# Performance work log

Measured on AMD Instinct MI355X. Metric: run time of the kernel, lower is better.

## Reference

```python
import jax, jax.numpy as jnp
import numpy as np

K = 3; STRIDE = 1; PAD = 1; DIL = 1; KN = K * K * K  # num_pts = 27


def _trilinear_sample(vol, grid):
    """F.grid_sample 3D, mode=bilinear, padding=zeros, align_corners=False.
    vol: (C, D, H, W); grid: (od, oh, ow, 3) with xyz order in [-1, 1].
    Returns (C, od, oh, ow)."""
    C, D, H, W = vol.shape
    # unnormalize (align_corners=False)
    ix = ((grid[..., 0] + 1.0) * W - 1.0) * 0.5
    iy = ((grid[..., 1] + 1.0) * H - 1.0) * 0.5
    iz = ((grid[..., 2] + 1.0) * D - 1.0) * 0.5
    x0 = jnp.floor(ix); y0 = jnp.floor(iy); z0 = jnp.floor(iz)
    out = jnp.zeros((C,) + grid.shape[:-1], vol.dtype)
    for dz in (0, 1):
        for dy in (0, 1):
            for dx in (0, 1):
                xc = x0 + dx; yc = y0 + dy; zc = z0 + dz
                w = (1.0 - jnp.abs(ix - xc)) * (1.0 - jnp.abs(iy - yc)) * (1.0 - jnp.abs(iz - zc))
                valid = (xc >= 0) & (xc < W) & (yc >= 0) & (yc < H) & (zc >= 0) & (zc < D)
                xi = jnp.clip(xc, 0, W - 1).astype(jnp.int32)
                yi = jnp.clip(yc, 0, H - 1).astype(jnp.int32)
                zi = jnp.clip(zc, 0, D - 1).astype(jnp.int32)
                val = vol[:, zi, yi, xi]  # (C, od, oh, ow)
                out = out + val * (w * valid.astype(vol.dtype))[None]
    return out


def setup_inputs() -> dict:
    key = jax.random.key(0)
    k1, k2, k3 = jax.random.split(key, 3)
    N, C, D, H, W = 2, 64, 16, 32, 32
    inp = jax.random.normal(k1, (N, C, D, H, W), dtype=jnp.float32)
    offset = jax.random.normal(k2, (N, KN * 3, D, H, W), dtype=jnp.float32)
    weight = jax.random.normal(k3, (64, 64, KN), dtype=jnp.float32) * 0.05
    return {"input": inp, "offset": offset, "weight": weight}


def reference(input, offset, weight):
    N, C, D, H, W = input.shape
    od, oh, ow = offset.shape[2], offset.shape[3], offset.shape[4]
    f32 = input.dtype
    # base sampling mesh (align_corners=True style normalization, as original)
    z = (jnp.arange(od) * STRIDE - PAD + ((K - 1) // 2) * DIL).astype(f32)
    y = (jnp.arange(oh) * STRIDE - PAD + ((K - 1) // 2) * DIL).astype(f32)
    x = (jnp.arange(ow) * STRIDE - PAD + ((K - 1) // 2) * DIL).astype(f32)
    mz, my, mx = jnp.meshgrid(z, y, x, indexing="ij")
    norm = lambda v, S: (v - (S - 1) / 2.0) / ((S - 1) / 2.0)
    mesh = jnp.stack([norm(mx, W), norm(my, H), norm(mz, D)], axis=-1)  # (od,oh,ow,3)
    # offsets: channel layout per kernel point is (dz, dy, dx)
    off = offset.reshape(N, KN, 3, od, oh, ow)
    goff = jnp.stack([
        off[:, :, 2] / ((W - 1) / 2.0),
        off[:, :, 1] / ((H - 1) / 2.0),
        off[:, :, 0] / ((D - 1) / 2.0),
    ], axis=-1)  # (N, KN, od, oh, ow, 3) xyz
    grid = mesh[None, None] + goff
    # per-batch, per-kernel-point trilinear gather -> (N, KN, C, od, oh, ow)
    sampled = jax.vmap(lambda v, g: jax.vmap(lambda gg: _trilinear_sample(v, gg))(g))(input, grid)
    # grouped matmul: weight (O, C, KN) flattened C-major matches sampled layout
    out = jnp.einsum("ock,nkcdhw->nodhw", weight, sampled)
    return out
```

## Files before the change

kernel.cpp:

```cpp
#include <hip/hip_runtime.h>

typedef __attribute__((ext_vector_type(8))) _Float16 half8;
typedef __attribute__((ext_vector_type(4))) float floatx4;

constexpr int NB  = 2;
constexpr int CC  = 64;
constexpr int DD  = 16;
constexpr int HH  = 32;
constexpr int WW  = 32;
constexpr int KN_ = 27;
constexpr int OC  = 64;
constexpr int DHW = DD * HH * WW;
constexpr int TP  = 16;
constexpr int KCH = 9;

__device__ __forceinline__ unsigned short f2h(float f) {
    _Float16 h = (_Float16)f;
    return *(unsigned short*)&h;
}

__global__ __launch_bounds__(256) void k_prep(const float* __restrict__ in,
                                              const float* __restrict__ w,
                                              unsigned int* __restrict__ outu,
                                              unsigned short* __restrict__ wf) {
    int bid = blockIdx.x;
    int t = threadIdx.x;
    if (bid < 512) {
        __shared__ float tile[64][65];
        int n  = bid >> 8;
        int v0 = (bid & 255) << 6;
        int lane = t & 63, row = t >> 6;
#pragma unroll
        for (int i = 0; i < 16; ++i) {
            int c = (i << 2) + row;
            tile[c][lane] = in[(size_t)(n * CC + c) * DHW + v0 + lane];
        }
        __syncthreads();
#pragma unroll
        for (int i = 0; i < 8; ++i) {
            int flat = i * 256 + t;
            int v = flat >> 5, cd = flat & 31;
            unsigned int lo = f2h(tile[2 * cd][v]);
            unsigned int hi = f2h(tile[2 * cd + 1][v]);
            outu[(size_t)(n * DHW + v0 + v) * 32 + cd] = lo | (hi << 16);
        }
    } else {
        int f = (bid - 512) * 256 + t;
        int i  = f & 7;
        int l  = (f >> 3) & 63;
        int ot = (f >> 9) & 3;
        int cc = (f >> 11) & 1;
        int k  = f >> 12;
        int o = ot * 16 + (l & 15);
        int c = cc * 32 + ((l >> 4) << 3) + i;
        wf[f] = f2h(w[(o * CC + c) * KN_ + k]);
    }
}

__global__ __launch_bounds__(128, 6) void k_main(const unsigned short* __restrict__ inp,
                                                 const unsigned short* __restrict__ wf,
                                                 const float* __restrict__ offs,
                                                 float* __restrict__ out) {
    __shared__ unsigned short S[2 * TP * 64];
    __shared__ unsigned int   SU[KCH * TP * 12];

    int t   = threadIdx.x;
    int bid = blockIdx.x;
    int n   = (bid >> 2) & 1;
    int idx = ((bid >> 3) << 2) | (bid & 3);
    int p0  = idx << 4;

    int sp = t >> 3;
    int cg = t & 7;
    int wv = t >> 6, l = t & 63;
    int lrow = l & 15, lk = l >> 4;

    const float* offb = offs + (size_t)n * (3 * KN_) * DHW + p0;
    const char*  inb  = (const char*)(inp + ((size_t)n * DHW << 6));

    floatx4 acc0 = {0.f, 0.f, 0.f, 0.f};
    floatx4 acc1 = {0.f, 0.f, 0.f, 0.f};

    const int cgo   = cg << 4;
    const int woff  = sp * 64 + ((cg ^ (sp & 7)) << 3);
    const int roff0 = lrow * 64 + (((0 | lk) ^ (lrow & 7)) << 3);
    const int roff1 = lrow * 64 + (((4 | lk) ^ (lrow & 7)) << 3);

    for (int ch = 0; ch < 3; ++ch) {
        __syncthreads();

        for (int si = t; si < KCH * TP; si += 128) {
            int kk = si >> 4, p = si & 15;
            int k  = ch * KCH + kk;
            int pa = p0 + p;
            int dpos = pa >> 10, hpos = (pa >> 5) & 31, wpos = pa & 31;

            float oz = offb[(k * 3 + 0) * DHW + p];
            float oy = offb[(k * 3 + 1) * DHW + p];
            float ox = offb[(k * 3 + 2) * DHW + p];
            float ix = ((float)wpos + ox) * (32.0f / 31.0f) - 0.5f;
            float iy = ((float)hpos + oy) * (32.0f / 31.0f) - 0.5f;
            float iz = ((float)dpos + oz) * (16.0f / 15.0f) - 0.5f;
            float xf = floorf(ix), yf = floorf(iy), zf = floorf(iz);
            float fx = ix - xf, fy = iy - yf, fz = iz - zf;
            int x0 = (int)xf, y0 = (int)yf, z0 = (int)zf;

            float wx0 = ((unsigned)x0       < (unsigned)WW) ? 1.f - fx : 0.f;
            float wx1 = ((unsigned)(x0 + 1) < (unsigned)WW) ? fx       : 0.f;
            float wy0 = ((unsigned)y0       < (unsigned)HH) ? 1.f - fy : 0.f;
            float wy1 = ((unsigned)(y0 + 1) < (unsigned)HH) ? fy       : 0.f;
            float wz0 = ((unsigned)z0       < (unsigned)DD) ? 1.f - fz : 0.f;
            float wz1 = ((unsigned)(z0 + 1) < (unsigned)DD) ? fz       : 0.f;

            int xc0 = min(max(x0, 0), WW - 1), xc1 = min(max(x0 + 1, 0), WW - 1);
            int yc0 = min(max(y0, 0), HH - 1), yc1 = min(max(y0 + 1, 0), HH - 1);
            int zc0 = min(max(z0, 0), DD - 1), zc1 = min(max(z0 + 1, 0), DD - 1);

            float wzy00 = wz0 * wy0, wzy01 = wz0 * wy1, wzy10 = wz1 * wy0, wzy11 = wz1 * wy1;
            unsigned int b00 = (zc0 * HH + yc0) * WW, b01 = (zc0 * HH + yc1) * WW;
            unsigned int b10 = (zc1 * HH + yc0) * WW, b11 = (zc1 * HH + yc1) * WW;

            uint4 vp, wp;
            vp.x = (b00 + xc0) | ((b00 + xc1) << 16);
            vp.y = (b01 + xc0) | ((b01 + xc1) << 16);
            vp.z = (b10 + xc0) | ((b10 + xc1) << 16);
            vp.w = (b11 + xc0) | ((b11 + xc1) << 16);
            wp.x = (unsigned int)f2h(wzy00 * wx0) | ((unsigned int)f2h(wzy00 * wx1) << 16);
            wp.y = (unsigned int)f2h(wzy01 * wx0) | ((unsigned int)f2h(wzy01 * wx1) << 16);
            wp.z = (unsigned int)f2h(wzy10 * wx0) | ((unsigned int)f2h(wzy10 * wx1) << 16);
            wp.w = (unsigned int)f2h(wzy11 * wx0) | ((unsigned int)f2h(wzy11 * wx1) << 16);

            unsigned int* rec = SU + si * 12;
            *(uint4*)rec       = vp;
            *(uint4*)(rec + 4) = wp;
        }
        __syncthreads();

        for (int kk = 0; kk < KCH; ++kk) {
            int k = ch * KCH + kk;

            const half8 wa00 = *(const half8*)(wf + ((((k << 1) | 0) * 4 + (wv << 1) + 0) << 9) + (l << 3));
            const half8 wa01 = *(const half8*)(wf + ((((k << 1) | 1) * 4 + (wv << 1) + 0) << 9) + (l << 3));
            const half8 wa10 = *(const half8*)(wf + ((((k << 1) | 0) * 4 + (wv << 1) + 1) << 9) + (l << 3));
            const half8 wa11 = *(const half8*)(wf + ((((k << 1) | 1) * 4 + (wv << 1) + 1) << 9) + (l << 3));

            const unsigned int* rec = SU + (kk * TP + sp) * 12;
            const uint4 vp = *(const uint4*)rec;
            const uint4 wp = *(const uint4*)(rec + 4);
            const unsigned int vpa[4] = {vp.x, vp.y, vp.z, vp.w};
            const unsigned int wpa[4] = {wp.x, wp.y, wp.z, wp.w};

            half8 accv = {0, 0, 0, 0, 0, 0, 0, 0};
#pragma unroll
            for (int cr = 0; cr < 8; ++cr) {
                unsigned int vd = vpa[cr >> 1];
                unsigned int wd = wpa[cr >> 1];
                unsigned int voxb = ((cr & 1) ? (vd >> 16) : (vd & 0xffffu)) << 7;
                unsigned short wu = (cr & 1) ? (unsigned short)(wd >> 16) : (unsigned short)wd;
                _Float16 wh = *(_Float16*)&wu;
                const half8 v = *(const half8*)(inb + voxb + cgo);
                half8 w8 = {wh, wh, wh, wh, wh, wh, wh, wh};
                accv += v * w8;
            }
            *(half8*)(S + ((k & 1) << 10) + woff) = accv;

            __syncthreads();

            const unsigned short* Sb = S + ((k & 1) << 10);
            const half8 bf0 = *(const half8*)(Sb + roff0);
            const half8 bf1 = *(const half8*)(Sb + roff1);
            acc0 = __builtin_amdgcn_mfma_f32_16x16x32_f16(wa00, bf0, acc0, 0, 0, 0);
            acc0 = __builtin_amdgcn_mfma_f32_16x16x32_f16(wa01, bf1, acc0, 0, 0, 0);
            acc1 = __builtin_amdgcn_mfma_f32_16x16x32_f16(wa10, bf0, acc1, 0, 0, 0);
            acc1 = __builtin_amdgcn_mfma_f32_16x16x32_f16(wa11, bf1, acc1, 0, 0, 0);
        }
    }

    float* ob = out + ((size_t)n * OC + (wv << 5) + (lk << 2)) * DHW + p0 + lrow;
#pragma unroll
    for (int r = 0; r < 4; ++r) {
        ob[r * DHW]              = acc0[r];
        ob[r * DHW + (DHW << 4)] = acc1[r];
    }
}

__global__ __launch_bounds__(256) void k_fallback(const float* __restrict__ inp,
                                                  const float* __restrict__ wt,
                                                  const float* __restrict__ offs,
                                                  float* __restrict__ out) {
    __shared__ float Slds[64][68];
    __shared__ float Wlds[64 * 64];
    int bid = blockIdx.x;
    int n = bid >> 8;
    int p0 = (bid & 255) * 64;
    int t = threadIdx.x;
    int cq = t & 15, c0 = cq << 2, pslot = t >> 4;
    int ob = (t & 15) << 2, pb = (t >> 4) << 2;
    int swz_w = (((cq & 7) ^ (cq >> 3)) << 2);
    float acc[4][4] = {};
    const float* offbase = offs + (size_t)n * (KN_ * 3) * DHW;
    for (int k = 0; k < KN_; ++k) {
#pragma unroll
        for (int i = 0; i < 16; ++i) {
            int f = i * 256 + t;
            int o = f & 63, c = f >> 6;
            Wlds[f] = wt[(o * CC + c) * KN_ + k];
        }
#pragma unroll
        for (int j = 0; j < 4; ++j) {
            int pl = pslot + 16 * j;
            int pa = p0 + pl;
            int d = pa >> 10, h = (pa >> 5) & 31, w = pa & 31;
            float offz = offbase[(k * 3 + 0) * DHW + pa];
            float offy = offbase[(k * 3 + 1) * DHW + pa];
            float offx = offbase[(k * 3 + 2) * DHW + pa];
            float ix = ((float)w + offx) * (32.0f / 31.0f) - 0.5f;
            float iy = ((float)h + offy) * (32.0f / 31.0f) - 0.5f;
            float iz = ((float)d + offz) * (16.0f / 15.0f) - 0.5f;
            float xf = floorf(ix), yf = floorf(iy), zf = floorf(iz);
            float fx = ix - xf, fy = iy - yf, fz = iz - zf;
            int x0 = (int)xf, y0 = (int)yf, z0 = (int)zf;
            float wx0 = 1.0f - fx, wx1 = fx, wy0 = 1.0f - fy, wy1 = fy, wz0 = 1.0f - fz, wz1 = fz;
            float s0 = 0.f, s1 = 0.f, s2 = 0.f, s3 = 0.f;
#pragma unroll
            for (int dz = 0; dz < 2; ++dz) {
                int zc = z0 + dz;
                if ((unsigned)zc >= (unsigned)DD) continue;
                float wz = dz ? wz1 : wz0;
#pragma unroll
                for (int dy = 0; dy < 2; ++dy) {
                    int yc = y0 + dy;
                    if ((unsigned)yc >= (unsigned)HH) continue;
                    float wzy = wz * (dy ? wy1 : wy0);
#pragma unroll
                    for (int dx = 0; dx < 2; ++dx) {
                        int xc = x0 + dx;
                        if ((unsigned)xc >= (unsigned)WW) continue;
                        float wf = wzy * (dx ? wx1 : wx0);
                        int vox = (zc * HH + yc) * WW + xc;
                        const float* b = inp + (size_t)(n * CC + c0) * DHW + vox;
                        s0 += wf * b[0]; s1 += wf * b[DHW];
                        s2 += wf * b[2 * DHW]; s3 += wf * b[3 * DHW];
                    }
                }
            }
            int plw = pl ^ swz_w;
            Slds[c0 + 0][plw] = s0; Slds[c0 + 1][plw] = s1;
            Slds[c0 + 2][plw] = s2; Slds[c0 + 3][plw] = s3;
        }
        __syncthreads();
#pragma unroll
        for (int c = 0; c < 64; ++c) {
            const int g = ((c >> 2) & 7) ^ (c >> 5);
            float4 wv = *(const float4*)(Wlds + c * 64 + ob);
            float4 sv = *(const float4*)(&Slds[c][pb ^ (g << 2)]);
            float wa[4] = {wv.x, wv.y, wv.z, wv.w};
            float sa[4] = {sv.x, sv.y, sv.z, sv.w};
#pragma unroll
            for (int i = 0; i < 4; ++i)
#pragma unroll
                for (int jj = 0; jj < 4; ++jj) acc[i][jj] += wa[i] * sa[jj];
        }
        __syncthreads();
    }
#pragma unroll
    for (int i = 0; i < 4; ++i) {
        float4 vv;
        vv.x = acc[i][0]; vv.y = acc[i][1]; vv.z = acc[i][2]; vv.w = acc[i][3];
        *(float4*)(out + (size_t)(n * OC + ob + i) * DHW + p0 + pb) = vv;
    }
}

extern "C" void kernel_launch(void* const* d_in, const int* in_sizes, int n_in,
                              void* d_out, int out_size, void* d_ws, size_t ws_size,
                              hipStream_t stream) {
    const float* inp = (const float*)d_in[0];
    const float* off = (const float*)d_in[1];
    const float* wgt = (const float*)d_in[2];
    float* out = (float*)d_out;

    const size_t in_f16_bytes = (size_t)NB * DHW * CC * 2;
    const size_t wf_bytes     = (size_t)KN_ * 2 * 4 * 64 * 8 * 2;

    if (ws_size >= in_f16_bytes + wf_bytes) {
        unsigned int*   in_t = (unsigned int*)d_ws;
        unsigned short* w_f  = (unsigned short*)((char*)d_ws + in_f16_bytes);
        k_prep<<<dim3(512 + 432), dim3(256), 0, stream>>>(inp, wgt, in_t, w_f);
        k_main<<<dim3(NB * 1024), dim3(128), 0, stream>>>(
            (const unsigned short*)in_t, w_f, off, out);
    } else {
        k_fallback<<<dim3(NB * 256), dim3(256), 0, stream>>>(inp, wgt, off, out);
    }
}
```

Baseline: 113.9 us.

## Software-pipeline trilinear gather with MFMA using 256-thread blocks and triple buffering

```diff
diff --git a/kernel.cpp b/kernel.cpp
--- a/kernel.cpp
+++ b/kernel.cpp
@@ -12,7 +12,6 @@
 constexpr int OC  = 64;
 constexpr int DHW = DD * HH * WW;
 constexpr int TP  = 16;
-constexpr int KCH = 9;
 
 __device__ __forceinline__ unsigned short f2h(float f) {
     _Float16 h = (_Float16)f;
@@ -57,12 +56,12 @@
     }
 }
 
-__global__ __launch_bounds__(128, 6) void k_main(const unsigned short* __restrict__ inp,
+__global__ __launch_bounds__(256, 5) void k_main(const unsigned short* __restrict__ inp,
                                                  const unsigned short* __restrict__ wf,
                                                  const float* __restrict__ offs,
                                                  float* __restrict__ out) {
-    __shared__ unsigned short S[2 * TP * 64];
-    __shared__ unsigned int   SU[KCH * TP * 12];
+    __shared__ unsigned short S[3 * TP * 64];
+    __shared__ unsigned int   SU[KN_ * TP * 8];
 
     int t   = threadIdx.x;
     int bid = blockIdx.x;
@@ -70,118 +69,153 @@
     int idx = ((bid >> 3) << 2) | (bid & 3);
     int p0  = idx << 4;
 
-    int sp = t >> 3;
-    int cg = t & 7;
-    int wv = t >> 6, l = t & 63;
+    int pair = t >> 7;
+    int tl   = t & 127;
+    int sp   = tl >> 3;
+    int cg   = tl & 7;
+
+    int w  = t >> 6;
+    int l  = t & 63;
     int lrow = l & 15, lk = l >> 4;
 
     const float* offb = offs + (size_t)n * (3 * KN_) * DHW + p0;
     const char*  inb  = (const char*)(inp + ((size_t)n * DHW << 6));
 
-    floatx4 acc0 = {0.f, 0.f, 0.f, 0.f};
-    floatx4 acc1 = {0.f, 0.f, 0.f, 0.f};
+    floatx4 acc = {0.f, 0.f, 0.f, 0.f};
 
     const int cgo   = cg << 4;
     const int woff  = sp * 64 + ((cg ^ (sp & 7)) << 3);
     const int roff0 = lrow * 64 + (((0 | lk) ^ (lrow & 7)) << 3);
     const int roff1 = lrow * 64 + (((4 | lk) ^ (lrow & 7)) << 3);
 
-    for (int ch = 0; ch < 3; ++ch) {
-        __syncthreads();
-
-        for (int si = t; si < KCH * TP; si += 128) {
-            int kk = si >> 4, p = si & 15;
-            int k  = ch * KCH + kk;
-            int pa = p0 + p;
-            int dpos = pa >> 10, hpos = (pa >> 5) & 31, wpos = pa & 31;
-
-            float oz = offb[(k * 3 + 0) * DHW + p];
-            float oy = offb[(k * 3 + 1) * DHW + p];
-            float ox = offb[(k * 3 + 2) * DHW + p];
-            float ix = ((float)wpos + ox) * (32.0f / 31.0f) - 0.5f;
-            float iy = ((float)hpos + oy) * (32.0f / 31.0f) - 0.5f;
-            float iz = ((float)dpos + oz) * (16.0f / 15.0f) - 0.5f;
-            float xf = floorf(ix), yf = floorf(iy), zf = floorf(iz);
-            float fx = ix - xf, fy = iy - yf, fz = iz - zf;
-            int x0 = (int)xf, y0 = (int)yf, z0 = (int)zf;
-
-            float wx0 = ((unsigned)x0       < (unsigned)WW) ? 1.f - fx : 0.f;
-            float wx1 = ((unsigned)(x0 + 1) < (unsigned)WW) ? fx       : 0.f;
-            float wy0 = ((unsigned)y0       < (unsigned)HH) ? 1.f - fy : 0.f;
-            float wy1 = ((unsigned)(y0 + 1) < (unsigned)HH) ? fy       : 0.f;
-            float wz0 = ((unsigned)z0       < (unsigned)DD) ? 1.f - fz : 0.f;
-            float wz1 = ((unsigned)(z0 + 1) < (unsigned)DD) ? fz       : 0.f;
-
-            int xc0 = min(max(x0, 0), WW - 1), xc1 = min(max(x0 + 1, 0), WW - 1);
-            int yc0 = min(max(y0, 0), HH - 1), yc1 = min(max(y0 + 1, 0), HH - 1);
-            int zc0 = min(max(z0, 0), DD - 1), zc1 = min(max(z0 + 1, 0), DD - 1);
-
-            float wzy00 = wz0 * wy0, wzy01 = wz0 * wy1, wzy10 = wz1 * wy0, wzy11 = wz1 * wy1;
-            unsigned int b00 = (zc0 * HH + yc0) * WW, b01 = (zc0 * HH + yc1) * WW;
-            unsigned int b10 = (zc1 * HH + yc0) * WW, b11 = (zc1 * HH + yc1) * WW;
-
-            uint4 vp, wp;
-            vp.x = (b00 + xc0) | ((b00 + xc1) << 16);
-            vp.y = (b01 + xc0) | ((b01 + xc1) << 16);
-            vp.z = (b10 + xc0) | ((b10 + xc1) << 16);
-            vp.w = (b11 + xc0) | ((b11 + xc1) << 16);
-            wp.x = (unsigned int)f2h(wzy00 * wx0) | ((unsigned int)f2h(wzy00 * wx1) << 16);
-            wp.y = (unsigned int)f2h(wzy01 * wx0) | ((unsigned int)f2h(wzy01 * wx1) << 16);
-            wp.z = (unsigned int)f2h(wzy10 * wx0) | ((unsigned int)f2h(wzy10 * wx1) << 16);
-            wp.w = (unsigned int)f2h(wzy11 * wx0) | ((unsigned int)f2h(wzy11 * wx1) << 16);
-
-            unsigned int* rec = SU + si * 12;
-            *(uint4*)rec       = vp;
-            *(uint4*)(rec + 4) = wp;
-        }
-        __syncthreads();
-
-        for (int kk = 0; kk < KCH; ++kk) {
-            int k = ch * KCH + kk;
-
-            const half8 wa00 = *(const half8*)(wf + ((((k << 1) | 0) * 4 + (wv << 1) + 0) << 9) + (l << 3));
-            const half8 wa01 = *(const half8*)(wf + ((((k << 1) | 1) * 4 + (wv << 1) + 0) << 9) + (l << 3));
-            const half8 wa10 = *(const half8*)(wf + ((((k << 1) | 0) * 4 + (wv << 1) + 1) << 9) + (l << 3));
-            const half8 wa11 = *(const half8*)(wf + ((((k << 1) | 1) * 4 + (wv << 1) + 1) << 9) + (l << 3));
-
-            const unsigned int* rec = SU + (kk * TP + sp) * 12;
+    for (int si = t; si < KN_ * TP; si += 256) {
+        int k = si >> 4, p = si & 15;
+        int pa = p0 + p;
+        int dpos = pa >> 10, hpos = (pa >> 5) & 31, wpos = pa & 31;
+
+        float oz = offb[(k * 3 + 0) * DHW + p];
+        float oy = offb[(k * 3 + 1) * DHW + p];
+        float ox = offb[(k * 3 + 2) * DHW + p];
+        float ix = ((float)wpos + ox) * (32.0f / 31.0f) - 0.5f;
+        float iy = ((float)hpos + oy) * (32.0f / 31.0f) - 0.5f;
+        float iz = ((float)dpos + oz) * (16.0f / 15.0f) - 0.5f;
+        float xf = floorf(ix), yf = floorf(iy), zf = floorf(iz);
+        float fx = ix - xf, fy = iy - yf, fz = iz - zf;
+        int x0 = (int)xf, y0 = (int)yf, z0 = (int)zf;
+
+        float wx0 = ((unsigned)x0       < (unsigned)WW) ? 1.f - fx : 0.f;
+        float wx1 = ((unsigned)(x0 + 1) < (unsigned)WW) ? fx       : 0.f;
+        float wy0 = ((unsigned)y0       < (unsigned)HH) ? 1.f - fy : 0.f;
+        float wy1 = ((unsigned)(y0 + 1) < (unsigned)HH) ? fy       : 0.f;
+        float wz0 = ((unsigned)z0       < (unsigned)DD) ? 1.f - fz : 0.f;
+        float wz1 = ((unsigned)(z0 + 1) < (unsigned)DD) ? fz       : 0.f;
+
+        int xc0 = min(max(x0, 0), WW - 1), xc1 = min(max(x0 + 1, 0), WW - 1);
+        int yc0 = min(max(y0, 0), HH - 1), yc1 = min(max(y0 + 1, 0), HH - 1);
+        int zc0 = min(max(z0, 0), DD - 1), zc1 = min(max(z0 + 1, 0), DD - 1);
+
+        float wzy00 = wz0 * wy0, wzy01 = wz0 * wy1, wzy10 = wz1 * wy0, wzy11 = wz1 * wy1;
+        unsigned int b00 = (zc0 * HH + yc0) * WW, b01 = (zc0 * HH + yc1) * WW;
+        unsigned int b10 = (zc1 * HH + yc0) * WW, b11 = (zc1 * HH + yc1) * WW;
+
+        uint4 vp, wp;
+        vp.x = (b00 + xc0) | ((b00 + xc1) << 16);
+        vp.y = (b01 + xc0) | ((b01 + xc1) << 16);
+        vp.z = (b10 + xc0) | ((b10 + xc1) << 16);
+        vp.w = (b11 + xc0) | ((b11 + xc1) << 16);
+        wp.x = (unsigned int)f2h(wzy00 * wx0) | ((unsigned int)f2h(wzy00 * wx1) << 16);
+        wp.y = (unsigned int)f2h(wzy01 * wx0) | ((unsigned int)f2h(wzy01 * wx1) << 16);
+        wp.z = (unsigned int)f2h(wzy10 * wx0) | ((unsigned int)f2h(wzy10 * wx1) << 16);
+        wp.w = (unsigned int)f2h(wzy11 * wx0) | ((unsigned int)f2h(wzy11 * wx1) << 16);
+
+        unsigned int* rec = SU + si * 8;
+        *(uint4*)rec       = vp;
+        *(uint4*)(rec + 4) = wp;
+    }
+
+    half8 wa0 = *(const half8*)(wf + (((0 * 2 + 0) * 4 + w) << 9) + (l << 3));
+    half8 wa1 = *(const half8*)(wf + (((0 * 2 + 1) * 4 + w) << 9) + (l << 3));
+
+    __syncthreads();
+
+    if (pair == 0) {
+        const unsigned int* rec = SU + sp * 8;
+        const uint4 vp = *(const uint4*)rec;
+        const uint4 wp = *(const uint4*)(rec + 4);
+        const unsigned int vpa[4] = {vp.x, vp.y, vp.z, vp.w};
+        const unsigned int wpa[4] = {wp.x, wp.y, wp.z, wp.w};
+        half8 accv = {0, 0, 0, 0, 0, 0, 0, 0};
+#pragma unroll
+        for (int cr = 0; cr < 8; ++cr) {
+            unsigned int vd = vpa[cr >> 1];
+            unsigned int wd = wpa[cr >> 1];
+            unsigned int voxb = ((cr & 1) ? (vd >> 16) : (vd & 0xffffu)) << 7;
+            unsigned short wu = (cr & 1) ? (unsigned short)(wd >> 16) : (unsigned short)wd;
+            _Float16 wh = *(_Float16*)&wu;
+            const half8 v = *(const half8*)(inb + voxb + cgo);
+            half8 w8 = {wh, wh, wh, wh, wh, wh, wh, wh};
+            accv += v * w8;
+        }
+        *(half8*)(S + woff) = accv;
+    }
+    __syncthreads();
+
+    int bc = 0;
+    for (int k = 0; k < KN_; ++k) {
+        const int kn = k + 1;
+        const int bn = (bc == 2) ? 0 : bc + 1;
+        const bool doS = (kn < KN_) && (pair == (kn & 1));
+
+        half8 g[8];
+        uint4 wp;
+        if (doS) {
+            const unsigned int* rec = SU + (kn * TP + sp) * 8;
             const uint4 vp = *(const uint4*)rec;
-            const uint4 wp = *(const uint4*)(rec + 4);
+            wp = *(const uint4*)(rec + 4);
             const unsigned int vpa[4] = {vp.x, vp.y, vp.z, vp.w};
-            const unsigned int wpa[4] = {wp.x, wp.y, wp.z, wp.w};
-
-            half8 accv = {0, 0, 0, 0, 0, 0, 0, 0};
 #pragma unroll
             for (int cr = 0; cr < 8; ++cr) {
                 unsigned int vd = vpa[cr >> 1];
+                unsigned int voxb = ((cr & 1) ? (vd >> 16) : (vd & 0xffffu)) << 7;
+                g[cr] = *(const half8*)(inb + voxb + cgo);
+            }
+        }
+
+        half8 nwa0 = wa0, nwa1 = wa1;
+        if (kn < KN_) {
+            nwa0 = *(const half8*)(wf + (((kn * 2 + 0) * 4 + w) << 9) + (l << 3));
+            nwa1 = *(const half8*)(wf + (((kn * 2 + 1) * 4 + w) << 9) + (l << 3));
+        }
+
+        const unsigned short* Sb = S + (bc << 10);
+        const half8 bf0 = *(const half8*)(Sb + roff0);
+        const half8 bf1 = *(const half8*)(Sb + roff1);
+        acc = __builtin_amdgcn_mfma_f32_16x16x32_f16(wa0, bf0, acc, 0, 0, 0);
+        acc = __builtin_amdgcn_mfma_f32_16x16x32_f16(wa1, bf1, acc, 0, 0, 0);
+
+        if (doS) {
+            const unsigned int wpa[4] = {wp.x, wp.y, wp.z, wp.w};
+            half8 accv = {0, 0, 0, 0, 0, 0, 0, 0};
+#pragma unroll
+            for (int cr = 0; cr < 8; ++cr) {
                 unsigned int wd = wpa[cr >> 1];
-                unsigned int voxb = ((cr & 1) ? (vd >> 16) : (vd & 0xffffu)) << 7;
                 unsigned short wu = (cr & 1) ? (unsigned short)(wd >> 16) : (unsigned short)wd;
                 _Float16 wh = *(_Float16*)&wu;
-                const half8 v = *(const half8*)(inb + voxb + cgo);
                 half8 w8 = {wh, wh, wh, wh, wh, wh, wh, wh};
-                accv += v * w8;
+                accv += g[cr] * w8;
             }
-            *(half8*)(S + ((k & 1) << 10) + woff) = accv;
-
-            __syncthreads();
-
-            const unsigned short* Sb = S + ((k & 1) << 10);
-            const half8 bf0 = *(const half8*)(Sb + roff0);
-            const half8 bf1 = *(const half8*)(Sb + roff1);
-            acc0 = __builtin_amdgcn_mfma_f32_16x16x32_f16(wa00, bf0, acc0, 0, 0, 0);
-            acc0 = __builtin_amdgcn_mfma_f32_16x16x32_f16(wa01, bf1, acc0, 0, 0, 0);
-            acc1 = __builtin_amdgcn_mfma_f32_16x16x32_f16(wa10, bf0, acc1, 0, 0, 0);
-            acc1 = __builtin_amdgcn_mfma_f32_16x16x32_f16(wa11, bf1, acc1, 0, 0, 0);
-        }
-    }
-
-    float* ob = out + ((size_t)n * OC + (wv << 5) + (lk << 2)) * DHW + p0 + lrow;
-#pragma unroll
-    for (int r = 0; r < 4; ++r) {
-        ob[r * DHW]              = acc0[r];
-        ob[r * DHW + (DHW << 4)] = acc1[r];
-    }
+            *(half8*)(S + (bn << 10) + woff) = accv;
+        }
+
+        wa0 = nwa0; wa1 = nwa1;
+        bc = bn;
+        __syncthreads();
+    }
+
+    float* ob = out + ((size_t)n * OC + (w << 4) + (lk << 2)) * DHW + p0 + lrow;
+#pragma unroll
+    for (int r = 0; r < 4; ++r)
+        ob[r * DHW] = acc[r];
 }
 
 __global__ __launch_bounds__(256) void k_fallback(const float* __restrict__ inp,
@@ -286,7 +320,7 @@
         unsigned int*   in_t = (unsigned int*)d_ws;
         unsigned short* w_f  = (unsigned short*)((char*)d_ws + in_f16_bytes);
         k_prep<<<dim3(512 + 432), dim3(256), 0, stream>>>(inp, wgt, in_t, w_f);
-        k_main<<<dim3(NB * 1024), dim3(128), 0, stream>>>(
+        k_main<<<dim3(2048), dim3(256), 0, stream>>>(
             (const unsigned short*)in_t, w_f, off, out);
     } else {
         k_fallback<<<dim3(NB * 256), dim3(256), 0, stream>>>(inp, wgt, off, out);
```

After: 118.9 us. 1.04x slower.

## Use single-wave blocks keeping gathered samples in registers for MFMA, dropping LDS staging

Applied to the files above, without the earlier changes.

```diff
diff --git a/kernel.cpp b/kernel.cpp
--- a/kernel.cpp
+++ b/kernel.cpp
@@ -12,7 +12,6 @@
 constexpr int OC  = 64;
 constexpr int DHW = DD * HH * WW;
 constexpr int TP  = 16;
-constexpr int KCH = 9;
 
 __device__ __forceinline__ unsigned short f2h(float f) {
     _Float16 h = (_Float16)f;
@@ -57,130 +56,126 @@
     }
 }
 
-__global__ __launch_bounds__(128, 6) void k_main(const unsigned short* __restrict__ inp,
-                                                 const unsigned short* __restrict__ wf,
-                                                 const float* __restrict__ offs,
-                                                 float* __restrict__ out) {
-    __shared__ unsigned short S[2 * TP * 64];
-    __shared__ unsigned int   SU[KCH * TP * 12];
-
-    int t   = threadIdx.x;
+__global__ __launch_bounds__(64, 2) void k_main(const unsigned short* __restrict__ inp,
+                                                const unsigned short* __restrict__ wf,
+                                                const float* __restrict__ offs,
+                                                float* __restrict__ out) {
+    __shared__ uint4 SUV[KN_ * TP];
+    __shared__ uint4 SUW[KN_ * TP];
+
+    int l   = threadIdx.x;
     int bid = blockIdx.x;
     int n   = (bid >> 2) & 1;
     int idx = ((bid >> 3) << 2) | (bid & 3);
     int p0  = idx << 4;
 
-    int sp = t >> 3;
-    int cg = t & 7;
-    int wv = t >> 6, l = t & 63;
-    int lrow = l & 15, lk = l >> 4;
-
     const float* offb = offs + (size_t)n * (3 * KN_) * DHW + p0;
     const char*  inb  = (const char*)(inp + ((size_t)n * DHW << 6));
 
+    for (int si = l; si < KN_ * TP; si += 64) {
+        int k = si >> 4, p = si & 15;
+        int pa = p0 + p;
+        int dpos = pa >> 10, hpos = (pa >> 5) & 31, wpos = pa & 31;
+
+        float oz = offb[(k * 3 + 0) * DHW + p];
+        float oy = offb[(k * 3 + 1) * DHW + p];
+        float ox = offb[(k * 3 + 2) * DHW + p];
+        float ix = ((float)wpos + ox) * (32.0f / 31.0f) - 0.5f;
+        float iy = ((float)hpos + oy) * (32.0f / 31.0f) - 0.5f;
+        float iz = ((float)dpos + oz) * (16.0f / 15.0f) - 0.5f;
+        float xf = floorf(ix), yf = floorf(iy), zf = floorf(iz);
+        float fx = ix - xf, fy = iy - yf, fz = iz - zf;
+        int x0 = (int)xf, y0 = (int)yf, z0 = (int)zf;
+
+        float wx0 = ((unsigned)x0       < (unsigned)WW) ? 1.f - fx : 0.f;
+        float wx1 = ((unsigned)(x0 + 1) < (unsigned)WW) ? fx       : 0.f;
+        float wy0 = ((unsigned)y0       < (unsigned)HH) ? 1.f - fy : 0.f;
+        float wy1 = ((unsigned)(y0 + 1) < (unsigned)HH) ? fy       : 0.f;
+        float wz0 = ((unsigned)z0       < (unsigned)DD) ? 1.f - fz : 0.f;
+        float wz1 = ((unsigned)(z0 + 1) < (unsigned)DD) ? fz       : 0.f;
+
+        int xc0 = min(max(x0, 0), WW - 1), xc1 = min(max(x0 + 1, 0), WW - 1);
+        int yc0 = min(max(y0, 0), HH - 1), yc1 = min(max(y0 + 1, 0), HH - 1);
+        int zc0 = min(max(z0, 0), DD - 1), zc1 = min(max(z0 + 1, 0), DD - 1);
+
+        float wzy00 = wz0 * wy0, wzy01 = wz0 * wy1, wzy10 = wz1 * wy0, wzy11 = wz1 * wy1;
+        unsigned int b00 = (zc0 * HH + yc0) * WW, b01 = (zc0 * HH + yc1) * WW;
+        unsigned int b10 = (zc1 * HH + yc0) * WW, b11 = (zc1 * HH + yc1) * WW;
+
+        uint4 vp, wp;
+        vp.x = (b00 + xc0) | ((b00 + xc1) << 16);
+        vp.y = (b01 + xc0) | ((b01 + xc1) << 16);
+        vp.z = (b10 + xc0) | ((b10 + xc1) << 16);
+        vp.w = (b11 + xc0) | ((b11 + xc1) << 16);
+        wp.x = (unsigned int)f2h(wzy00 * wx0) | ((unsigned int)f2h(wzy00 * wx1) << 16);
+        wp.y = (unsigned int)f2h(wzy01 * wx0) | ((unsigned int)f2h(wzy01 * wx1) << 16);
+        wp.z = (unsigned int)f2h(wzy10 * wx0) | ((unsigned int)f2h(wzy10 * wx1) << 16);
+        wp.w = (unsigned int)f2h(wzy11 * wx0) | ((unsigned int)f2h(wzy11 * wx1) << 16);
+
+        SUV[si] = vp;
+        SUW[si] = wp;
+    }
+    __syncthreads();
+
+    const int prow = l & 15;
+    const int cp   = l >> 4;
+    const int cpo  = cp << 4;
+
     floatx4 acc0 = {0.f, 0.f, 0.f, 0.f};
     floatx4 acc1 = {0.f, 0.f, 0.f, 0.f};
-
-    const int cgo   = cg << 4;
-    const int woff  = sp * 64 + ((cg ^ (sp & 7)) << 3);
-    const int roff0 = lrow * 64 + (((0 | lk) ^ (lrow & 7)) << 3);
-    const int roff1 = lrow * 64 + (((4 | lk) ^ (lrow & 7)) << 3);
-
-    for (int ch = 0; ch < 3; ++ch) {
-        __syncthreads();
-
-        for (int si = t; si < KCH * TP; si += 128) {
-            int kk = si >> 4, p = si & 15;
-            int k  = ch * KCH + kk;
-            int pa = p0 + p;
-            int dpos = pa >> 10, hpos = (pa >> 5) & 31, wpos = pa & 31;
-
-            float oz = offb[(k * 3 + 0) * DHW + p];
-            float oy = offb[(k * 3 + 1) * DHW + p];
-            float ox = offb[(k * 3 + 2) * DHW + p];
-            float ix = ((float)wpos + ox) * (32.0f / 31.0f) - 0.5f;
-            float iy = ((float)hpos + oy) * (32.0f / 31.0f) - 0.5f;
-            float iz = ((float)dpos + oz) * (16.0f / 15.0f) - 0.5f;
-            float xf = floorf(ix), yf = floorf(iy), zf = floorf(iz);
-            float fx = ix - xf, fy = iy - yf, fz = iz - zf;
-            int x0 = (int)xf, y0 = (int)yf, z0 = (int)zf;
-
-            float wx0 = ((unsigned)x0       < (unsigned)WW) ? 1.f - fx : 0.f;
-            float wx1 = ((unsigned)(x0 + 1) < (unsigned)WW) ? fx       : 0.f;
-            float wy0 = ((unsigned)y0       < (unsigned)HH) ? 1.f - fy : 0.f;
-            float wy1 = ((unsigned)(y0 + 1) < (unsigned)HH) ? fy       : 0.f;
-            float wz0 = ((unsigned)z0       < (unsigned)DD) ? 1.f - fz : 0.f;
-            float wz1 = ((unsigned)(z0 + 1) < (unsigned)DD) ? fz       : 0.f;
-
-            int xc0 = min(max(x0, 0), WW - 1), xc1 = min(max(x0 + 1, 0), WW - 1);
-            int yc0 = min(max(y0, 0), HH - 1), yc1 = min(max(y0 + 1, 0), HH - 1);
-            int zc0 = min(max(z0, 0), DD - 1), zc1 = min(max(z0 + 1, 0), DD - 1);
-
-            float wzy00 = wz0 * wy0, wzy01 = wz0 * wy1, wzy10 = wz1 * wy0, wzy11 = wz1 * wy1;
-            unsigned int b00 = (zc0 * HH + yc0) * WW, b01 = (zc0 * HH + yc1) * WW;
-            unsigned int b10 = (zc1 * HH + yc0) * WW, b11 = (zc1 * HH + yc1) * WW;
-
-            uint4 vp, wp;
-            vp.x = (b00 + xc0) | ((b00 + xc1) << 16);
-            vp.y = (b01 + xc0) | ((b01 + xc1) << 16);
-            vp.z = (b10 + xc0) | ((b10 + xc1) << 16);
-            vp.w = (b11 + xc0) | ((b11 + xc1) << 16);
-            wp.x = (unsigned int)f2h(wzy00 * wx0) | ((unsigned int)f2h(wzy00 * wx1) << 16);
-            wp.y = (unsigned int)f2h(wzy01 * wx0) | ((unsigned int)f2h(wzy01 * wx1) << 16);
-            wp.z = (unsigned int)f2h(wzy10 * wx0) | ((unsigned int)f2h(wzy10 * wx1) << 16);
-            wp.w = (unsigned int)f2h(wzy11 * wx0) | ((unsigned int)f2h(wzy11 * wx1) << 16);
-
-            unsigned int* rec = SU + si * 12;
-            *(uint4*)rec       = vp;
-            *(uint4*)(rec + 4) = wp;
-        }
-        __syncthreads();
-
-        for (int kk = 0; kk < KCH; ++kk) {
-            int k = ch * KCH + kk;
-
-            const half8 wa00 = *(const half8*)(wf + ((((k << 1) | 0) * 4 + (wv << 1) + 0) << 9) + (l << 3));
-            const half8 wa01 = *(const half8*)(wf + ((((k << 1) | 1) * 4 + (wv << 1) + 0) << 9) + (l << 3));
-            const half8 wa10 = *(const half8*)(wf + ((((k << 1) | 0) * 4 + (wv << 1) + 1) << 9) + (l << 3));
-            const half8 wa11 = *(const half8*)(wf + ((((k << 1) | 1) * 4 + (wv << 1) + 1) << 9) + (l << 3));
-
-            const unsigned int* rec = SU + (kk * TP + sp) * 12;
-            const uint4 vp = *(const uint4*)rec;
-            const uint4 wp = *(const uint4*)(rec + 4);
-            const unsigned int vpa[4] = {vp.x, vp.y, vp.z, vp.w};
-            const unsigned int wpa[4] = {wp.x, wp.y, wp.z, wp.w};
-
-            half8 accv = {0, 0, 0, 0, 0, 0, 0, 0};
-#pragma unroll
-            for (int cr = 0; cr < 8; ++cr) {
-                unsigned int vd = vpa[cr >> 1];
-                unsigned int wd = wpa[cr >> 1];
-                unsigned int voxb = ((cr & 1) ? (vd >> 16) : (vd & 0xffffu)) << 7;
-                unsigned short wu = (cr & 1) ? (unsigned short)(wd >> 16) : (unsigned short)wd;
-                _Float16 wh = *(_Float16*)&wu;
-                const half8 v = *(const half8*)(inb + voxb + cgo);
-                half8 w8 = {wh, wh, wh, wh, wh, wh, wh, wh};
-                accv += v * w8;
-            }
-            *(half8*)(S + ((k & 1) << 10) + woff) = accv;
-
-            __syncthreads();
-
-            const unsigned short* Sb = S + ((k & 1) << 10);
-            const half8 bf0 = *(const half8*)(Sb + roff0);
-            const half8 bf1 = *(const half8*)(Sb + roff1);
-            acc0 = __builtin_amdgcn_mfma_f32_16x16x32_f16(wa00, bf0, acc0, 0, 0, 0);
-            acc0 = __builtin_amdgcn_mfma_f32_16x16x32_f16(wa01, bf1, acc0, 0, 0, 0);
-            acc1 = __builtin_amdgcn_mfma_f32_16x16x32_f16(wa10, bf0, acc1, 0, 0, 0);
-            acc1 = __builtin_amdgcn_mfma_f32_16x16x32_f16(wa11, bf1, acc1, 0, 0, 0);
-        }
-    }
-
-    float* ob = out + ((size_t)n * OC + (wv << 5) + (lk << 2)) * DHW + p0 + lrow;
+    floatx4 acc2 = {0.f, 0.f, 0.f, 0.f};
+    floatx4 acc3 = {0.f, 0.f, 0.f, 0.f};
+
+    for (int k = 0; k < KN_; ++k) {
+        const uint4 vp = SUV[(k << 4) + prow];
+        const uint4 wp = SUW[(k << 4) + prow];
+        const unsigned int vpa[4] = {vp.x, vp.y, vp.z, vp.w};
+        const unsigned int wpa[4] = {wp.x, wp.y, wp.z, wp.w};
+
+        const unsigned short* wfk = wf + ((size_t)(k << 3) << 9) + (l << 3);
+        half8 wa0 = *(const half8*)(wfk);
+        half8 wa1 = *(const half8*)(wfk + (1 << 9));
+        half8 wa2 = *(const half8*)(wfk + (2 << 9));
+        half8 wa3 = *(const half8*)(wfk + (3 << 9));
+        half8 wb0 = *(const half8*)(wfk + (4 << 9));
+        half8 wb1 = *(const half8*)(wfk + (5 << 9));
+        half8 wb2 = *(const half8*)(wfk + (6 << 9));
+        half8 wb3 = *(const half8*)(wfk + (7 << 9));
+
+        half8 a0 = {0, 0, 0, 0, 0, 0, 0, 0};
+        half8 a1 = {0, 0, 0, 0, 0, 0, 0, 0};
+#pragma unroll
+        for (int cr = 0; cr < 8; ++cr) {
+            unsigned int vd = vpa[cr >> 1];
+            unsigned int voxb = ((cr & 1) ? (vd >> 16) : (vd & 0xffffu)) << 7;
+            const char* base = inb + voxb + cpo;
+            const half8 v0 = *(const half8*)(base);
+            const half8 v1 = *(const half8*)(base + 64);
+            unsigned int wd = wpa[cr >> 1];
+            unsigned short wu = (cr & 1) ? (unsigned short)(wd >> 16) : (unsigned short)wd;
+            _Float16 wh = *(_Float16*)&wu;
+            half8 w8 = {wh, wh, wh, wh, wh, wh, wh, wh};
+            a0 += v0 * w8;
+            a1 += v1 * w8;
+        }
+
+        acc0 = __builtin_amdgcn_mfma_f32_16x16x32_f16(wa0, a0, acc0, 0, 0, 0);
+        acc0 = __builtin_amdgcn_mfma_f32_16x16x32_f16(wb0, a1, acc0, 0, 0, 0);
+        acc1 = __builtin_amdgcn_mfma_f32_16x16x32_f16(wa1, a0, acc1, 0, 0, 0);
+        acc1 = __builtin_amdgcn_mfma_f32_16x16x32_f16(wb1, a1, acc1, 0, 0, 0);
+        acc2 = __builtin_amdgcn_mfma_f32_16x16x32_f16(wa2, a0, acc2, 0, 0, 0);
+        acc2 = __builtin_amdgcn_mfma_f32_16x16x32_f16(wb2, a1, acc2, 0, 0, 0);
+        acc3 = __builtin_amdgcn_mfma_f32_16x16x32_f16(wa3, a0, acc3, 0, 0, 0);
+        acc3 = __builtin_amdgcn_mfma_f32_16x16x32_f16(wb3, a1, acc3, 0, 0, 0);
+    }
+
+    float* ob = out + (size_t)n * OC * DHW + p0 + prow + (size_t)(cp << 2) * DHW;
 #pragma unroll
     for (int r = 0; r < 4; ++r) {
-        ob[r * DHW]              = acc0[r];
-        ob[r * DHW + (DHW << 4)] = acc1[r];
+        ob[(size_t)(r +  0) * DHW] = acc0[r];
+        ob[(size_t)(r + 16) * DHW] = acc1[r];
+        ob[(size_t)(r + 32) * DHW] = acc2[r];
+        ob[(size_t)(r + 48) * DHW] = acc3[r];
     }
 }
 
@@ -286,7 +281,7 @@
         unsigned int*   in_t = (unsigned int*)d_ws;
         unsigned short* w_f  = (unsigned short*)((char*)d_ws + in_f16_bytes);
         k_prep<<<dim3(512 + 432), dim3(256), 0, stream>>>(inp, wgt, in_t, w_f);
-        k_main<<<dim3(NB * 1024), dim3(128), 0, stream>>>(
+        k_main<<<dim3(2048), dim3(64), 0, stream>>>(
             (const unsigned short*)in_t, w_f, off, out);
     } else {
         k_fallback<<<dim3(NB * 256), dim3(256), 0, stream>>>(inp, wgt, off, out);
```

Measured after the change: 181.7 us. 1.6x slower.

## Split kernel-point reduction across two blocks with atomic accumulation into zeroed output

Applied to the files above, without the earlier changes.

```diff
diff --git a/kernel.cpp b/kernel.cpp
--- a/kernel.cpp
+++ b/kernel.cpp
@@ -9,10 +9,10 @@
 constexpr int HH  = 32;
 constexpr int WW  = 32;
 constexpr int KN_ = 27;
+constexpr int KSP = 14;
 constexpr int OC  = 64;
 constexpr int DHW = DD * HH * WW;
 constexpr int TP  = 16;
-constexpr int KCH = 9;
 
 __device__ __forceinline__ unsigned short f2h(float f) {
     _Float16 h = (_Float16)f;
@@ -22,7 +22,8 @@
 __global__ __launch_bounds__(256) void k_prep(const float* __restrict__ in,
                                               const float* __restrict__ w,
                                               unsigned int* __restrict__ outu,
-                                              unsigned short* __restrict__ wf) {
+                                              unsigned short* __restrict__ wf,
+                                              float4* __restrict__ outz) {
     int bid = blockIdx.x;
     int t = threadIdx.x;
     if (bid < 512) {
@@ -44,7 +45,7 @@
             unsigned int hi = f2h(tile[2 * cd + 1][v]);
             outu[(size_t)(n * DHW + v0 + v) * 32 + cd] = lo | (hi << 16);
         }
-    } else {
+    } else if (bid < 944) {
         int f = (bid - 512) * 256 + t;
         int i  = f & 7;
         int l  = (f >> 3) & 63;
@@ -54,25 +55,33 @@
         int o = ot * 16 + (l & 15);
         int c = cc * 32 + ((l >> 4) << 3) + i;
         wf[f] = f2h(w[(o * CC + c) * KN_ + k]);
-    }
-}
-
-__global__ __launch_bounds__(128, 6) void k_main(const unsigned short* __restrict__ inp,
+    } else {
+        float4 z = {0.f, 0.f, 0.f, 0.f};
+        outz[(bid - 944) * 256 + t] = z;
+    }
+}
+
+__global__ __launch_bounds__(128, 8) void k_main(const unsigned short* __restrict__ inp,
                                                  const unsigned short* __restrict__ wf,
                                                  const float* __restrict__ offs,
                                                  float* __restrict__ out) {
     __shared__ unsigned short S[2 * TP * 64];
-    __shared__ unsigned int   SU[KCH * TP * 12];
+    __shared__ uint4 SUV[KSP * TP];
+    __shared__ uint4 SUW[KSP * TP];
 
     int t   = threadIdx.x;
     int bid = blockIdx.x;
     int n   = (bid >> 2) & 1;
-    int idx = ((bid >> 3) << 2) | (bid & 3);
+    int h   = (bid >> 3) & 1;
+    int idx = ((bid >> 4) << 2) | (bid & 3);
     int p0  = idx << 4;
+    int k0  = h ? KSP : 0;
+    int nk  = h ? (KN_ - KSP) : KSP;
 
     int sp = t >> 3;
     int cg = t & 7;
-    int wv = t >> 6, l = t & 63;
+    int wv = t >> 6;
+    int l  = t & 63;
     int lrow = l & 15, lk = l >> 4;
 
     const float* offb = offs + (size_t)n * (3 * KN_) * DHW + p0;
@@ -86,101 +95,95 @@
     const int roff0 = lrow * 64 + (((0 | lk) ^ (lrow & 7)) << 3);
     const int roff1 = lrow * 64 + (((4 | lk) ^ (lrow & 7)) << 3);
 
-    for (int ch = 0; ch < 3; ++ch) {
-        __syncthreads();
-
-        for (int si = t; si < KCH * TP; si += 128) {
-            int kk = si >> 4, p = si & 15;
-            int k  = ch * KCH + kk;
-            int pa = p0 + p;
-            int dpos = pa >> 10, hpos = (pa >> 5) & 31, wpos = pa & 31;
-
-            float oz = offb[(k * 3 + 0) * DHW + p];
-            float oy = offb[(k * 3 + 1) * DHW + p];
-            float ox = offb[(k * 3 + 2) * DHW + p];
-            float ix = ((float)wpos + ox) * (32.0f / 31.0f) - 0.5f;
-            float iy = ((float)hpos + oy) * (32.0f / 31.0f) - 0.5f;
-            float iz = ((float)dpos + oz) * (16.0f / 15.0f) - 0.5f;
-            float xf = floorf(ix), yf = floorf(iy), zf = floorf(iz);
-            float fx = ix - xf, fy = iy - yf, fz = iz - zf;
-            int x0 = (int)xf, y0 = (int)yf, z0 = (int)zf;
-
-            float wx0 = ((unsigned)x0       < (unsigned)WW) ? 1.f - fx : 0.f;
-            float wx1 = ((unsigned)(x0 + 1) < (unsigned)WW) ? fx       : 0.f;
-            float wy0 = ((unsigned)y0       < (unsigned)HH) ? 1.f - fy : 0.f;
-            float wy1 = ((unsigned)(y0 + 1) < (unsigned)HH) ? fy       : 0.f;
-            float wz0 = ((unsigned)z0       < (unsigned)DD) ? 1.f - fz : 0.f;
-            float wz1 = ((unsigned)(z0 + 1) < (unsigned)DD) ? fz       : 0.f;
-
-            int xc0 = min(max(x0, 0), WW - 1), xc1 = min(max(x0 + 1, 0), WW - 1);
-            int yc0 = min(max(y0, 0), HH - 1), yc1 = min(max(y0 + 1, 0), HH - 1);
-            int zc0 = min(max(z0, 0), DD - 1), zc1 = min(max(z0 + 1, 0), DD - 1);
-
-            float wzy00 = wz0 * wy0, wzy01 = wz0 * wy1, wzy10 = wz1 * wy0, wzy11 = wz1 * wy1;
-            unsigned int b00 = (zc0 * HH + yc0) * WW, b01 = (zc0 * HH + yc1) * WW;
-            unsigned int b10 = (zc1 * HH + yc0) * WW, b11 = (zc1 * HH + yc1) * WW;
-
-            uint4 vp, wp;
-            vp.x = (b00 + xc0) | ((b00 + xc1) << 16);
-            vp.y = (b01 + xc0) | ((b01 + xc1) << 16);
-            vp.z = (b10 + xc0) | ((b10 + xc1) << 16);
-            vp.w = (b11 + xc0) | ((b11 + xc1) << 16);
-            wp.x = (unsigned int)f2h(wzy00 * wx0) | ((unsigned int)f2h(wzy00 * wx1) << 16);
-            wp.y = (unsigned int)f2h(wzy01 * wx0) | ((unsigned int)f2h(wzy01 * wx1) << 16);
-            wp.z = (unsigned int)f2h(wzy10 * wx0) | ((unsigned int)f2h(wzy10 * wx1) << 16);
-            wp.w = (unsigned int)f2h(wzy11 * wx0) | ((unsigned int)f2h(wzy11 * wx1) << 16);
-
-            unsigned int* rec = SU + si * 12;
-            *(uint4*)rec       = vp;
-            *(uint4*)(rec + 4) = wp;
-        }
-        __syncthreads();
-
-        for (int kk = 0; kk < KCH; ++kk) {
-            int k = ch * KCH + kk;
-
-            const half8 wa00 = *(const half8*)(wf + ((((k << 1) | 0) * 4 + (wv << 1) + 0) << 9) + (l << 3));
-            const half8 wa01 = *(const half8*)(wf + ((((k << 1) | 1) * 4 + (wv << 1) + 0) << 9) + (l << 3));
-            const half8 wa10 = *(const half8*)(wf + ((((k << 1) | 0) * 4 + (wv << 1) + 1) << 9) + (l << 3));
-            const half8 wa11 = *(const half8*)(wf + ((((k << 1) | 1) * 4 + (wv << 1) + 1) << 9) + (l << 3));
-
-            const unsigned int* rec = SU + (kk * TP + sp) * 12;
-            const uint4 vp = *(const uint4*)rec;
-            const uint4 wp = *(const uint4*)(rec + 4);
-            const unsigned int vpa[4] = {vp.x, vp.y, vp.z, vp.w};
-            const unsigned int wpa[4] = {wp.x, wp.y, wp.z, wp.w};
-
-            half8 accv = {0, 0, 0, 0, 0, 0, 0, 0};
-#pragma unroll
-            for (int cr = 0; cr < 8; ++cr) {
-                unsigned int vd = vpa[cr >> 1];
-                unsigned int wd = wpa[cr >> 1];
-                unsigned int voxb = ((cr & 1) ? (vd >> 16) : (vd & 0xffffu)) << 7;
-                unsigned short wu = (cr & 1) ? (unsigned short)(wd >> 16) : (unsigned short)wd;
-                _Float16 wh = *(_Float16*)&wu;
-                const half8 v = *(const half8*)(inb + voxb + cgo);
-                half8 w8 = {wh, wh, wh, wh, wh, wh, wh, wh};
-                accv += v * w8;
-            }
-            *(half8*)(S + ((k & 1) << 10) + woff) = accv;
-
-            __syncthreads();
-
-            const unsigned short* Sb = S + ((k & 1) << 10);
-            const half8 bf0 = *(const half8*)(Sb + roff0);
-            const half8 bf1 = *(const half8*)(Sb + roff1);
-            acc0 = __builtin_amdgcn_mfma_f32_16x16x32_f16(wa00, bf0, acc0, 0, 0, 0);
-            acc0 = __builtin_amdgcn_mfma_f32_16x16x32_f16(wa01, bf1, acc0, 0, 0, 0);
-            acc1 = __builtin_amdgcn_mfma_f32_16x16x32_f16(wa10, bf0, acc1, 0, 0, 0);
-            acc1 = __builtin_amdgcn_mfma_f32_16x16x32_f16(wa11, bf1, acc1, 0, 0, 0);
-        }
+    for (int si = t; si < nk * TP; si += 128) {
+        int krel = si >> 4, p = si & 15;
+        int k  = k0 + krel;
+        int pa = p0 + p;
+        int dpos = pa >> 10, hpos = (pa >> 5) & 31, wpos = pa & 31;
+
+        float oz = offb[(k * 3 + 0) * DHW + p];
+        float oy = offb[(k * 3 + 1) * DHW + p];
+        float ox = offb[(k * 3 + 2) * DHW + p];
+        float ix = ((float)wpos + ox) * (32.0f / 31.0f) - 0.5f;
+        float iy = ((float)hpos + oy) * (32.0f / 31.0f) - 0.5f;
+        float iz = ((float)dpos + oz) * (16.0f / 15.0f) - 0.5f;
+        float xf = floorf(ix), yf = floorf(iy), zf = floorf(iz);
+        float fx = ix - xf, fy = iy - yf, fz = iz - zf;
+        int x0 = (int)xf, y0 = (int)yf, z0 = (int)zf;
+
+        float wx0 = ((unsigned)x0       < (unsigned)WW) ? 1.f - fx : 0.f;
+        float wx1 = ((unsigned)(x0 + 1) < (unsigned)WW) ? fx       : 0.f;
+        float wy0 = ((unsigned)y0       < (unsigned)HH) ? 1.f - fy : 0.f;
+        float wy1 = ((unsigned)(y0 + 1) < (unsigned)HH) ? fy       : 0.f;
+        float wz0 = ((unsigned)z0       < (unsigned)DD) ? 1.f - fz : 0.f;
+        float wz1 = ((unsigned)(z0 + 1) < (unsigned)DD) ? fz       : 0.f;
+
+        int xc0 = min(max(x0, 0), WW - 1), xc1 = min(max(x0 + 1, 0), WW - 1);
+        int yc0 = min(max(y0, 0), HH - 1), yc1 = min(max(y0 + 1, 0), HH - 1);
+        int zc0 = min(max(z0, 0), DD - 1), zc1 = min(max(z0 + 1, 0), DD - 1);
+
+        float wzy00 = wz0 * wy0, wzy01 = wz0 * wy1, wzy10 = wz1 * wy0, wzy11 = wz1 * wy1;
+        unsigned int b00 = (zc0 * HH + yc0) * WW, b01 = (zc0 * HH + yc1) * WW;
+        unsigned int b10 = (zc1 * HH + yc0) * WW, b11 = (zc1 * HH + yc1) * WW;
+
+        uint4 vp, wp;
+        vp.x = (b00 + xc0) | ((b00 + xc1) << 16);
+        vp.y = (b01 + xc0) | ((b01 + xc1) << 16);
+        vp.z = (b10 + xc0) | ((b10 + xc1) << 16);
+        vp.w = (b11 + xc0) | ((b11 + xc1) << 16);
+        wp.x = (unsigned int)f2h(wzy00 * wx0) | ((unsigned int)f2h(wzy00 * wx1) << 16);
+        wp.y = (unsigned int)f2h(wzy01 * wx0) | ((unsigned int)f2h(wzy01 * wx1) << 16);
+        wp.z = (unsigned int)f2h(wzy10 * wx0) | ((unsigned int)f2h(wzy10 * wx1) << 16);
+        wp.w = (unsigned int)f2h(wzy11 * wx0) | ((unsigned int)f2h(wzy11 * wx1) << 16);
+
+        SUV[si] = vp;
+        SUW[si] = wp;
+    }
+    __syncthreads();
+
+    for (int krel = 0; krel < nk; ++krel) {
+        int k = k0 + krel;
+
+        const half8 wa00 = *(const half8*)(wf + ((((k << 1) | 0) * 4 + (wv << 1) + 0) << 9) + (l << 3));
+        const half8 wa01 = *(const half8*)(wf + ((((k << 1) | 1) * 4 + (wv << 1) + 0) << 9) + (l << 3));
+        const half8 wa10 = *(const half8*)(wf + ((((k << 1) | 0) * 4 + (wv << 1) + 1) << 9) + (l << 3));
+        const half8 wa11 = *(const half8*)(wf + ((((k << 1) | 1) * 4 + (wv << 1) + 1) << 9) + (l << 3));
+
+        const uint4 vp = SUV[(krel << 4) + sp];
+        const uint4 wp = SUW[(krel << 4) + sp];
+        const unsigned int vpa[4] = {vp.x, vp.y, vp.z, vp.w};
+        const unsigned int wpa[4] = {wp.x, wp.y, wp.z, wp.w};
+
+        half8 accv = {0, 0, 0, 0, 0, 0, 0, 0};
+#pragma unroll
+        for (int cr = 0; cr < 8; ++cr) {
+            unsigned int vd = vpa[cr >> 1];
+            unsigned int voxb = ((cr & 1) ? (vd >> 16) : (vd & 0xffffu)) << 7;
+            unsigned int wd = wpa[cr >> 1];
+            unsigned short wu = (cr & 1) ? (unsigned short)(wd >> 16) : (unsigned short)wd;
+            _Float16 wh = *(_Float16*)&wu;
+            const half8 v = *(const half8*)(inb + voxb + cgo);
+            half8 w8 = {wh, wh, wh, wh, wh, wh, wh, wh};
+            accv += v * w8;
+        }
+        *(half8*)(S + ((krel & 1) << 10) + woff) = accv;
+
+        __syncthreads();
+
+        const unsigned short* Sb = S + ((krel & 1) << 10);
+        const half8 bf0 = *(const half8*)(Sb + roff0);
+        const half8 bf1 = *(const half8*)(Sb + roff1);
+        acc0 = __builtin_amdgcn_mfma_f32_16x16x32_f16(wa00, bf0, acc0, 0, 0, 0);
+        acc0 = __builtin_amdgcn_mfma_f32_16x16x32_f16(wa01, bf1, acc0, 0, 0, 0);
+        acc1 = __builtin_amdgcn_mfma_f32_16x16x32_f16(wa10, bf0, acc1, 0, 0, 0);
+        acc1 = __builtin_amdgcn_mfma_f32_16x16x32_f16(wa11, bf1, acc1, 0, 0, 0);
     }
 
     float* ob = out + ((size_t)n * OC + (wv << 5) + (lk << 2)) * DHW + p0 + lrow;
 #pragma unroll
     for (int r = 0; r < 4; ++r) {
-        ob[r * DHW]              = acc0[r];
-        ob[r * DHW + (DHW << 4)] = acc1[r];
+        atomicAdd(&ob[r * DHW], acc0[r]);
+        atomicAdd(&ob[r * DHW + (DHW << 4)], acc1[r]);
     }
 }
 
@@ -285,8 +288,9 @@
     if (ws_size >= in_f16_bytes + wf_bytes) {
         unsigned int*   in_t = (unsigned int*)d_ws;
         unsigned short* w_f  = (unsigned short*)((char*)d_ws + in_f16_bytes);
-        k_prep<<<dim3(512 + 432), dim3(256), 0, stream>>>(inp, wgt, in_t, w_f);
-        k_main<<<dim3(NB * 1024), dim3(128), 0, stream>>>(
+        k_prep<<<dim3(512 + 432 + 2048), dim3(256), 0, stream>>>(
+            inp, wgt, in_t, w_f, (float4*)out);
+        k_main<<<dim3(4096), dim3(128), 0, stream>>>(
             (const unsigned short*)in_t, w_f, off, out);
     } else {
         k_fallback<<<dim3(NB * 256), dim3(256), 0, stream>>>(inp, wgt, off, out);
```

Result: slower. 119.9 us (+5.3%).
